# Performance work log

Measured on AMD Instinct MI355X. Metric: run time of the kernel, lower is better.

Reference implementation:

```python
import jax, jax.numpy as jnp
import numpy as np

B, S, HID = 2, 2048, 768
NH, HD = 12, 64  # num heads, head dim


def setup_inputs() -> dict:
    key = jax.random.key(0)
    ks = jax.random.split(key, 10)
    scale = 0.02
    return {
        "hidden_states": jax.random.normal(ks[0], (B, S, HID), jnp.float32),
        "rel_pos": jax.random.normal(ks[1], (B, NH, S, S), jnp.float32),
        "rel_2d_pos": jax.random.normal(ks[2], (B, NH, S, S), jnp.float32),
        "attention_mask": jax.random.randint(ks[3], (B, 1, S, S), 0, 2, jnp.int32),
        "Wq": jax.random.normal(ks[4], (HID, HID), jnp.float32) * scale,
        "bq": jnp.zeros((HID,), jnp.float32),
        "Wk": jax.random.normal(ks[5], (HID, HID), jnp.float32) * scale,
        "bk": jnp.zeros((HID,), jnp.float32),
        "Wv": jax.random.normal(ks[6], (HID, HID), jnp.float32) * scale,
        "bv": jnp.zeros((HID,), jnp.float32),
    }


def _heads(x):
    # [B,S,HID] -> [B,NH,S,HD]
    return x.reshape(B, S, NH, HD).transpose(0, 2, 1, 3)


def reference(hidden_states, rel_pos, rel_2d_pos, attention_mask, Wq, bq, Wk, bk, Wv, bv):
    q = _heads(hidden_states @ Wq.T + bq) / jnp.sqrt(jnp.asarray(HD, hidden_states.dtype))
    k = _heads(hidden_states @ Wk.T + bk)
    v = _heads(hidden_states @ Wv.T + bv)
    scores = jnp.einsum('bhsd,bhtd->bhst', q, k)
    scores = scores + rel_pos + rel_2d_pos
    scores = jnp.where(attention_mask.astype(bool), jnp.finfo(jnp.float32).min, scores.astype(jnp.float32))
    probs = jax.nn.softmax(scores, axis=-1).astype(v.dtype)
    ctx = jnp.einsum('bhst,bhtd->bhsd', probs, v)
    return ctx.transpose(0, 2, 1, 3).reshape(B, S, HID)
```

## Files before the change

### kernel.cpp

```cpp
#include <hip/hip_runtime.h>

#define B_ 2
#define S_ 2048
#define HID_ 768
#define NH_ 12
#define HD_ 64

typedef unsigned short u16;
typedef __attribute__((ext_vector_type(8))) short bf16x8;
typedef __attribute__((ext_vector_type(4))) float f32x4;

static __device__ inline u16 f2bf(float f) {
    union { float f; unsigned u; } v; v.f = f;
    unsigned r = v.u + 0x7fffu + ((v.u >> 16) & 1u);
    return (u16)(r >> 16);
}

__global__ void cast_bf16(const float* __restrict__ src, u16* __restrict__ dst, int n) {
    int i = (blockIdx.x * blockDim.x + threadIdx.x) * 4;
    if (i < n) {
        float4 v = *(const float4*)(src + i);
        unsigned lo = (unsigned)f2bf(v.x) | ((unsigned)f2bf(v.y) << 16);
        unsigned hi = (unsigned)f2bf(v.z) | ((unsigned)f2bf(v.w) << 16);
        uint2 o; o.x = lo; o.y = hi;
        *(uint2*)(dst + i) = o;
    }
}

__global__ __launch_bounds__(256) void qkv_gemm(
    const u16* __restrict__ hsb, const u16* __restrict__ wcat,
    const float* __restrict__ bq, const float* __restrict__ bk, const float* __restrict__ bv,
    u16* __restrict__ Qg, u16* __restrict__ Kg, u16* __restrict__ Vtg)
{
    __shared__ u16 As[64 * 40];
    __shared__ u16 Bs[64 * 40];
    __shared__ u16 Vs[64 * 72];

    const int m0 = blockIdx.x * 64;
    const int n0 = blockIdx.y * 64;
    const int tid = threadIdx.x;
    const int wave = tid >> 6, lane = tid & 63;
    const int l = lane & 15, quad = lane >> 4;

    f32x4 acc[4];
#pragma unroll
    for (int t = 0; t < 4; t++) acc[t] = (f32x4){0.f, 0.f, 0.f, 0.f};

    const int srow = tid >> 2;
    const int skg = (tid & 3) * 8;

    for (int k0 = 0; k0 < HID_; k0 += 32) {
        *(int4*)(&As[srow * 40 + skg]) = *(const int4*)(&hsb[(size_t)(m0 + srow) * HID_ + k0 + skg]);
        *(int4*)(&Bs[srow * 40 + skg]) = *(const int4*)(&wcat[(size_t)(n0 + srow) * HID_ + k0 + skg]);
        __syncthreads();
        bf16x8 a = *(const bf16x8*)(&As[(wave * 16 + l) * 40 + quad * 8]);
#pragma unroll
        for (int t = 0; t < 4; t++) {
            bf16x8 b = *(const bf16x8*)(&Bs[(t * 16 + l) * 40 + quad * 8]);
            acc[t] = __builtin_amdgcn_mfma_f32_16x16x32_bf16(a, b, acc[t], 0, 0, 0);
        }
        __syncthreads();
    }

    const int proj = n0 / HID_;
    const int cbase = n0 - proj * HID_;
    const int h = cbase >> 6;
    const int bidx = m0 >> 11;
    const int srow0 = m0 & (S_ - 1);
    const float* bias = (proj == 0) ? bq : ((proj == 1) ? bk : bv);

    if (proj < 2) {
        u16* dst = (proj == 0) ? Qg : Kg;
        const float sc = (proj == 0) ? 0.125f : 1.0f;
#pragma unroll
        for (int t = 0; t < 4; t++) {
            const int d = t * 16 + l;
            const float bb = bias[cbase + d];
#pragma unroll
            for (int rr = 0; rr < 4; rr++) {
                int s = srow0 + wave * 16 + quad * 4 + rr;
                float v = (acc[t][rr] + bb) * sc;
                dst[(((size_t)bidx * NH_ + h) * S_ + s) * HD_ + d] = f2bf(v);
            }
        }
    } else {
#pragma unroll
        for (int t = 0; t < 4; t++) {
            const int d = t * 16 + l;
            const float bb = bias[cbase + d];
#pragma unroll
            for (int rr = 0; rr < 4; rr++) {
                int sl = wave * 16 + quad * 4 + rr;
                Vs[d * 72 + sl] = f2bf(acc[t][rr] + bb);
            }
        }
        __syncthreads();
        const int drow = tid >> 2;
        const int sseg = (tid & 3) * 16;
        size_t base = (((size_t)bidx * NH_ + h) * HD_ + drow) * S_ + srow0 + sseg;
        *(int4*)(&Vtg[base])     = *(const int4*)(&Vs[drow * 72 + sseg]);
        *(int4*)(&Vtg[base + 8]) = *(const int4*)(&Vs[drow * 72 + sseg + 8]);
    }
}

__global__ __launch_bounds__(256) void attn(
    const u16* __restrict__ Qg, const u16* __restrict__ Kg, const u16* __restrict__ Vtg,
    const float* __restrict__ rel, const float* __restrict__ rel2,
    const int* __restrict__ mask, float* __restrict__ out)
{
    __shared__ u16 Ks[64 * 72];
    __shared__ u16 Vts[64 * 72];
    __shared__ u16 Ps[4 * 16 * 72];

    const int q0 = blockIdx.x * 64;
    const int h = blockIdx.y;
    const int b = blockIdx.z;
    const int tid = threadIdx.x;
    const int wave = tid >> 6, lane = tid & 63;
    const int l = lane & 15, quad = lane >> 4;
    const int bh = b * NH_ + h;

    bf16x8 qf[2];
    {
        const int qrow = q0 + wave * 16 + l;
        qf[0] = *(const bf16x8*)(&Qg[((size_t)bh * S_ + qrow) * HD_ + quad * 8]);
        qf[1] = *(const bf16x8*)(&Qg[((size_t)bh * S_ + qrow) * HD_ + 32 + quad * 8]);
    }

    f32x4 o[4];
#pragma unroll
    for (int t = 0; t < 4; t++) o[t] = (f32x4){0.f, 0.f, 0.f, 0.f};
    float m_run[4], l_run[4];
#pragma unroll
    for (int rr = 0; rr < 4; rr++) { m_run[rr] = -3.4028234663852886e38f; l_run[rr] = 0.f; }

    const int srow = tid >> 2;
    const int sseg = (tid & 3) * 8;

    const size_t relbase = (size_t)bh * S_ * S_;
    const size_t mbase = (size_t)b * S_ * S_;

    for (int k0 = 0; k0 < S_; k0 += 64) {
        {
            size_t kg = ((size_t)bh * S_ + k0 + srow) * HD_;
            *(int4*)(&Ks[srow * 72 + sseg])      = *(const int4*)(&Kg[kg + sseg]);
            *(int4*)(&Ks[srow * 72 + 32 + sseg]) = *(const int4*)(&Kg[kg + 32 + sseg]);
            size_t vg = ((size_t)bh * HD_ + srow) * S_ + k0;
            *(int4*)(&Vts[srow * 72 + sseg])      = *(const int4*)(&Vtg[vg + sseg]);
            *(int4*)(&Vts[srow * 72 + 32 + sseg]) = *(const int4*)(&Vtg[vg + 32 + sseg]);
        }
        __syncthreads();

        f32x4 sacc[4];
#pragma unroll
        for (int t = 0; t < 4; t++) {
            const int col = k0 + t * 16 + l;
#pragma unroll
            for (int rr = 0; rr < 4; rr++) {
                const int row = q0 + wave * 16 + quad * 4 + rr;
                sacc[t][rr] = rel[relbase + (size_t)row * S_ + col] +
                              rel2[relbase + (size_t)row * S_ + col];
            }
            bf16x8 b0 = *(const bf16x8*)(&Ks[(t * 16 + l) * 72 + quad * 8]);
            sacc[t] = __builtin_amdgcn_mfma_f32_16x16x32_bf16(qf[0], b0, sacc[t], 0, 0, 0);
            bf16x8 b1 = *(const bf16x8*)(&Ks[(t * 16 + l) * 72 + 32 + quad * 8]);
            sacc[t] = __builtin_amdgcn_mfma_f32_16x16x32_bf16(qf[1], b1, sacc[t], 0, 0, 0);
#pragma unroll
            for (int rr = 0; rr < 4; rr++) {
                const int row = q0 + wave * 16 + quad * 4 + rr;
                if (mask[mbase + (size_t)row * S_ + col])
                    sacc[t][rr] = -3.4028234663852886e38f;
            }
        }

#pragma unroll
        for (int rr = 0; rr < 4; rr++) {
            float mx = fmaxf(fmaxf(sacc[0][rr], sacc[1][rr]), fmaxf(sacc[2][rr], sacc[3][rr]));
#pragma unroll
            for (int off = 1; off < 16; off <<= 1) mx = fmaxf(mx, __shfl_xor(mx, off, 64));
            float mnew = fmaxf(m_run[rr], mx);
            float alpha = __expf(m_run[rr] - mnew);
            float rs = 0.f;
#pragma unroll
            for (int t = 0; t < 4; t++) {
                float p = __expf(sacc[t][rr] - mnew);
                sacc[t][rr] = p;
                rs += p;
            }
#pragma unroll
            for (int off = 1; off < 16; off <<= 1) rs += __shfl_xor(rs, off, 64);
            l_run[rr] = l_run[rr] * alpha + rs;
            m_run[rr] = mnew;
#pragma unroll
            for (int dt = 0; dt < 4; dt++) o[dt][rr] *= alpha;
        }

#pragma unroll
        for (int t = 0; t < 4; t++)
#pragma unroll
            for (int rr = 0; rr < 4; rr++)
                Ps[(wave * 16 + quad * 4 + rr) * 72 + t * 16 + l] = f2bf(sacc[t][rr]);
        __syncthreads();

        bf16x8 pa0 = *(const bf16x8*)(&Ps[(wave * 16 + l) * 72 + quad * 8]);
        bf16x8 pa1 = *(const bf16x8*)(&Ps[(wave * 16 + l) * 72 + 32 + quad * 8]);
#pragma unroll
        for (int dt = 0; dt < 4; dt++) {
            bf16x8 v0 = *(const bf16x8*)(&Vts[(dt * 16 + l) * 72 + quad * 8]);
            o[dt] = __builtin_amdgcn_mfma_f32_16x16x32_bf16(pa0, v0, o[dt], 0, 0, 0);
            bf16x8 v1 = *(const bf16x8*)(&Vts[(dt * 16 + l) * 72 + 32 + quad * 8]);
            o[dt] = __builtin_amdgcn_mfma_f32_16x16x32_bf16(pa1, v1, o[dt], 0, 0, 0);
        }
        __syncthreads();
    }

#pragma unroll
    for (int dt = 0; dt < 4; dt++) {
#pragma unroll
        for (int rr = 0; rr < 4; rr++) {
            const int row = q0 + wave * 16 + quad * 4 + rr;
            out[((size_t)b * S_ + row) * HID_ + h * HD_ + dt * 16 + l] = o[dt][rr] / l_run[rr];
        }
    }
}

extern "C" void kernel_launch(void* const* d_in, const int* in_sizes, int n_in,
                              void* d_out, int out_size, void* d_ws, size_t ws_size,
                              hipStream_t stream) {
    const float* hs   = (const float*)d_in[0];
    const float* rel  = (const float*)d_in[1];
    const float* rel2 = (const float*)d_in[2];
    const int*   mask = (const int*)d_in[3];
    const float* Wq = (const float*)d_in[4];
    const float* bq = (const float*)d_in[5];
    const float* Wk = (const float*)d_in[6];
    const float* bk = (const float*)d_in[7];
    const float* Wv = (const float*)d_in[8];
    const float* bv = (const float*)d_in[9];
    float* out = (float*)d_out;

    char* ws = (char*)d_ws;
    u16* hsb  = (u16*)(ws);
    u16* wcat = (u16*)(ws + 6291456);
    u16* Qg   = (u16*)(ws + 9830400);
    u16* Kg   = (u16*)(ws + 16121856);
    u16* Vtg  = (u16*)(ws + 22413312);

    cast_bf16<<<3072, 256, 0, stream>>>(hs, hsb, B_ * S_ * HID_);
    cast_bf16<<<576, 256, 0, stream>>>(Wq, wcat,             HID_ * HID_);
    cast_bf16<<<576, 256, 0, stream>>>(Wk, wcat + HID_ * HID_,     HID_ * HID_);
    cast_bf16<<<576, 256, 0, stream>>>(Wv, wcat + 2 * HID_ * HID_, HID_ * HID_);

    qkv_gemm<<<dim3(64, 36), 256, 0, stream>>>(hsb, wcat, bq, bk, bv, Qg, Kg, Vtg);

    attn<<<dim3(S_ / 64, NH_, B_), 256, 0, stream>>>(Qg, Kg, Vtg, rel, rel2, mask, out);
}
```

Measured before the change: 875.7 us.

## Transpose QK^T MFMA for row-contiguous bias loads and prefetch next tile

Swaps the MFMA operands so each lane holds one query row with four contiguous key columns. This lets rel_pos, rel_2d_pos and mask be read as float4/int4 vectors instead of scattered scalar loads. Bias and mask for the next key tile are prefetched into registers, and K/V global loads are issued before the LDS stores so their latency overlaps compute. The softmax reductions shrink to two cross-quad shuffles with per-row scalar stats, and P is written as packed uint2. The cost is more live registers and extra shuffles to broadcast alpha and l back to the output layout.

After: 918.6 us. 4.9% more time.

```diff
diff --git a/kernel.cpp b/kernel.cpp
--- a/kernel.cpp
+++ b/kernel.cpp
@@ -120,6 +120,8 @@
     const int l = lane & 15, quad = lane >> 4;
     const int bh = b * NH_ + h;
 
+    const float NEG = -3.4028234663852886e38f;
+
     bf16x8 qf[2];
     {
         const int qrow = q0 + wave * 16 + l;
@@ -130,76 +132,105 @@
     f32x4 o[4];
 #pragma unroll
     for (int t = 0; t < 4; t++) o[t] = (f32x4){0.f, 0.f, 0.f, 0.f};
-    float m_run[4], l_run[4];
-#pragma unroll
-    for (int rr = 0; rr < 4; rr++) { m_run[rr] = -3.4028234663852886e38f; l_run[rr] = 0.f; }
+    float m_run = NEG, l_run = 0.f;
 
     const int srow = tid >> 2;
     const int sseg = (tid & 3) * 8;
 
-    const size_t relbase = (size_t)bh * S_ * S_;
-    const size_t mbase = (size_t)b * S_ * S_;
+    const int qrow = q0 + wave * 16 + l;
+    const float* relR  = rel  + (size_t)bh * S_ * S_ + (size_t)qrow * S_;
+    const float* rel2R = rel2 + (size_t)bh * S_ * S_ + (size_t)qrow * S_;
+    const int*   maskR = mask + (size_t)b * S_ * S_ + (size_t)qrow * S_;
+
+    float4 pr1[4], pr2[4];
+    int4 pmk[4];
+#pragma unroll
+    for (int t = 0; t < 4; t++) {
+        const int c = t * 16 + quad * 4;
+        pr1[t] = *(const float4*)(relR + c);
+        pr2[t] = *(const float4*)(rel2R + c);
+        pmk[t] = *(const int4*)(maskR + c);
+    }
 
     for (int k0 = 0; k0 < S_; k0 += 64) {
-        {
-            size_t kg = ((size_t)bh * S_ + k0 + srow) * HD_;
-            *(int4*)(&Ks[srow * 72 + sseg])      = *(const int4*)(&Kg[kg + sseg]);
-            *(int4*)(&Ks[srow * 72 + 32 + sseg]) = *(const int4*)(&Kg[kg + 32 + sseg]);
-            size_t vg = ((size_t)bh * HD_ + srow) * S_ + k0;
-            *(int4*)(&Vts[srow * 72 + sseg])      = *(const int4*)(&Vtg[vg + sseg]);
-            *(int4*)(&Vts[srow * 72 + 32 + sseg]) = *(const int4*)(&Vtg[vg + 32 + sseg]);
-        }
-        __syncthreads();
+        size_t kg = ((size_t)bh * S_ + k0 + srow) * HD_;
+        int4 ka = *(const int4*)(&Kg[kg + sseg]);
+        int4 kb = *(const int4*)(&Kg[kg + 32 + sseg]);
+        size_t vg = ((size_t)bh * HD_ + srow) * S_ + k0;
+        int4 va = *(const int4*)(&Vtg[vg + sseg]);
+        int4 vb = *(const int4*)(&Vtg[vg + 32 + sseg]);
 
         f32x4 sacc[4];
 #pragma unroll
         for (int t = 0; t < 4; t++) {
-            const int col = k0 + t * 16 + l;
+            sacc[t][0] = pmk[t].x ? NEG : pr1[t].x + pr2[t].x;
+            sacc[t][1] = pmk[t].y ? NEG : pr1[t].y + pr2[t].y;
+            sacc[t][2] = pmk[t].z ? NEG : pr1[t].z + pr2[t].z;
+            sacc[t][3] = pmk[t].w ? NEG : pr1[t].w + pr2[t].w;
+        }
+
+        if (k0 + 64 < S_) {
+#pragma unroll
+            for (int t = 0; t < 4; t++) {
+                const int c = k0 + 64 + t * 16 + quad * 4;
+                pr1[t] = *(const float4*)(relR + c);
+                pr2[t] = *(const float4*)(rel2R + c);
+                pmk[t] = *(const int4*)(maskR + c);
+            }
+        }
+
+        *(int4*)(&Ks[srow * 72 + sseg])       = ka;
+        *(int4*)(&Ks[srow * 72 + 32 + sseg])  = kb;
+        *(int4*)(&Vts[srow * 72 + sseg])      = va;
+        *(int4*)(&Vts[srow * 72 + 32 + sseg]) = vb;
+        __syncthreads();
+
+#pragma unroll
+        for (int t = 0; t < 4; t++) {
+            bf16x8 b0 = *(const bf16x8*)(&Ks[(t * 16 + l) * 72 + quad * 8]);
+            sacc[t] = __builtin_amdgcn_mfma_f32_16x16x32_bf16(b0, qf[0], sacc[t], 0, 0, 0);
+            bf16x8 b1 = *(const bf16x8*)(&Ks[(t * 16 + l) * 72 + 32 + quad * 8]);
+            sacc[t] = __builtin_amdgcn_mfma_f32_16x16x32_bf16(b1, qf[1], sacc[t], 0, 0, 0);
+        }
+
+        float mx = NEG;
+#pragma unroll
+        for (int t = 0; t < 4; t++)
+#pragma unroll
+            for (int rr = 0; rr < 4; rr++) mx = fmaxf(mx, sacc[t][rr]);
+        mx = fmaxf(mx, __shfl_xor(mx, 16, 64));
+        mx = fmaxf(mx, __shfl_xor(mx, 32, 64));
+        float mnew = fmaxf(m_run, mx);
+        float alpha = __expf(m_run - mnew);
+        float rs = 0.f;
+#pragma unroll
+        for (int t = 0; t < 4; t++)
 #pragma unroll
             for (int rr = 0; rr < 4; rr++) {
-                const int row = q0 + wave * 16 + quad * 4 + rr;
-                sacc[t][rr] = rel[relbase + (size_t)row * S_ + col] +
-                              rel2[relbase + (size_t)row * S_ + col];
-            }
-            bf16x8 b0 = *(const bf16x8*)(&Ks[(t * 16 + l) * 72 + quad * 8]);
-            sacc[t] = __builtin_amdgcn_mfma_f32_16x16x32_bf16(qf[0], b0, sacc[t], 0, 0, 0);
-            bf16x8 b1 = *(const bf16x8*)(&Ks[(t * 16 + l) * 72 + 32 + quad * 8]);
-            sacc[t] = __builtin_amdgcn_mfma_f32_16x16x32_bf16(qf[1], b1, sacc[t], 0, 0, 0);
-#pragma unroll
-            for (int rr = 0; rr < 4; rr++) {
-                const int row = q0 + wave * 16 + quad * 4 + rr;
-                if (mask[mbase + (size_t)row * S_ + col])
-                    sacc[t][rr] = -3.4028234663852886e38f;
-            }
-        }
-
-#pragma unroll
-        for (int rr = 0; rr < 4; rr++) {
-            float mx = fmaxf(fmaxf(sacc[0][rr], sacc[1][rr]), fmaxf(sacc[2][rr], sacc[3][rr]));
-#pragma unroll
-            for (int off = 1; off < 16; off <<= 1) mx = fmaxf(mx, __shfl_xor(mx, off, 64));
-            float mnew = fmaxf(m_run[rr], mx);
-            float alpha = __expf(m_run[rr] - mnew);
-            float rs = 0.f;
-#pragma unroll
-            for (int t = 0; t < 4; t++) {
                 float p = __expf(sacc[t][rr] - mnew);
                 sacc[t][rr] = p;
                 rs += p;
             }
-#pragma unroll
-            for (int off = 1; off < 16; off <<= 1) rs += __shfl_xor(rs, off, 64);
-            l_run[rr] = l_run[rr] * alpha + rs;
-            m_run[rr] = mnew;
-#pragma unroll
-            for (int dt = 0; dt < 4; dt++) o[dt][rr] *= alpha;
-        }
-
-#pragma unroll
-        for (int t = 0; t < 4; t++)
-#pragma unroll
-            for (int rr = 0; rr < 4; rr++)
-                Ps[(wave * 16 + quad * 4 + rr) * 72 + t * 16 + l] = f2bf(sacc[t][rr]);
+        rs += __shfl_xor(rs, 16, 64);
+        rs += __shfl_xor(rs, 32, 64);
+        l_run = l_run * alpha + rs;
+        m_run = mnew;
+
+        float av[4];
+#pragma unroll
+        for (int rr = 0; rr < 4; rr++) av[rr] = __shfl(alpha, quad * 4 + rr, 64);
+#pragma unroll
+        for (int dt = 0; dt < 4; dt++)
+#pragma unroll
+            for (int rr = 0; rr < 4; rr++) o[dt][rr] *= av[rr];
+
+#pragma unroll
+        for (int t = 0; t < 4; t++) {
+            unsigned p01 = (unsigned)f2bf(sacc[t][0]) | ((unsigned)f2bf(sacc[t][1]) << 16);
+            unsigned p23 = (unsigned)f2bf(sacc[t][2]) | ((unsigned)f2bf(sacc[t][3]) << 16);
+            uint2 pw; pw.x = p01; pw.y = p23;
+            *(uint2*)(&Ps[(wave * 16 + l) * 72 + t * 16 + quad * 4]) = pw;
+        }
         __syncthreads();
 
         bf16x8 pa0 = *(const bf16x8*)(&Ps[(wave * 16 + l) * 72 + quad * 8]);
@@ -214,12 +245,15 @@
         __syncthreads();
     }
 
+    float lv[4];
+#pragma unroll
+    for (int rr = 0; rr < 4; rr++) lv[rr] = __shfl(l_run, quad * 4 + rr, 64);
 #pragma unroll
     for (int dt = 0; dt < 4; dt++) {
 #pragma unroll
         for (int rr = 0; rr < 4; rr++) {
             const int row = q0 + wave * 16 + quad * 4 + rr;
-            out[((size_t)b * S_ + row) * HID_ + h * HD_ + dt * 16 + l] = o[dt][rr] / l_run[rr];
+            out[((size_t)b * S_ + row) * HID_ + h * HD_ + dt * 16 + l] = o[dt][rr] / lv[rr];
         }
     }
 }
```
